# Kernel tuning notes

Measured on AMD Instinct MI355X. Metric: run time of the kernel, lower is better.

Reference implementation:

```python
import jax, jax.numpy as jnp
import numpy as np
import math

EMBED_DIM = 1024
MEMORY_DIM = 1024
MEMORY_SIZE = 2048
B, S = 8, 4096


def bitnet_linear(x, W, b):
    """Eval-mode BitNetLinear: 1.58-bit weight quant + 8-bit activation quant."""
    w_scale = jnp.mean(jnp.abs(W))
    qW = jnp.sign(W) * (jnp.abs(W) > 0.5 * w_scale).astype(W.dtype)
    i_scale = jnp.max(jnp.abs(x)) / 127.0
    qx = jnp.clip(jnp.round(x / i_scale), -128.0, 127.0)
    out = jnp.einsum('bsi,oi->bso', qx, qW) * (w_scale * i_scale)
    return out + b


def setup_inputs() -> dict:
    key = jax.random.key(0)
    ks = jax.random.split(key, 9)
    return {
        'x': jax.random.normal(ks[0], (B, S, EMBED_DIM), jnp.float32),
        'memory_keys': jax.random.normal(ks[1], (MEMORY_SIZE, MEMORY_DIM), jnp.float32),
        'memory_values': jax.random.normal(ks[2], (MEMORY_SIZE, EMBED_DIM), jnp.float32),
        'Wk': jax.random.normal(ks[3], (MEMORY_DIM, EMBED_DIM), jnp.float32) * 0.1,
        'bk': jnp.zeros((MEMORY_DIM,), jnp.float32),
        'Wv': jax.random.normal(ks[4], (EMBED_DIM, EMBED_DIM), jnp.float32) * 0.1,
        'bv': jnp.zeros((EMBED_DIM,), jnp.float32),
        'Wo': jax.random.normal(ks[5], (EMBED_DIM, EMBED_DIM), jnp.float32) * 0.1,
        'bo': jnp.zeros((EMBED_DIM,), jnp.float32),
    }


def reference(x, memory_keys, memory_values, Wk, bk, Wv, bv, Wo, bo):
    # quantized key/value projections
    query_keys = bitnet_linear(x, Wk, bk)          # [B, S, Dm]
    _query_values = bitnet_linear(x, Wv, bv)       # computed in original (used only by update path)
    # memory cross-attention over fixed bank
    similarities = jnp.einsum('bsd,md->bsm', query_keys, memory_keys)  # [B, S, M]
    attention_weights = jax.nn.softmax(similarities / math.sqrt(MEMORY_DIM), axis=-1)
    retrieved = jnp.einsum('bsm,me->bse', attention_weights, memory_values)  # [B, S, E]
    output = bitnet_linear(x + retrieved, Wo, bo)
    return output
```

## Files before the change

### kernel.cpp

```cpp
#include <hip/hip_runtime.h>
#include <hip/hip_bf16.h>
#include <stdint.h>
#include <type_traits>

typedef __attribute__((ext_vector_type(8))) short bf16x8;
typedef __attribute__((ext_vector_type(4))) float f32x4;
typedef __attribute__((ext_vector_type(4))) int i32x4;

struct Scalars {
  double sum_wk;
  double sum_wo;
  unsigned int max_x_bits;
  unsigned int max_y_bits;
};

__device__ __forceinline__ unsigned short f2bf(float f) {
  __hip_bfloat16 h = __float2bfloat16(f);
  return *reinterpret_cast<unsigned short*>(&h);
}

__device__ __forceinline__ void async16(void* lds, const void* g) {
  __builtin_amdgcn_global_load_lds((__attribute__((address_space(1))) void*)g,
                                   (__attribute__((address_space(3))) void*)lds, 16, 0, 0);
}

__device__ __forceinline__ void tile_swizzle(int nxShift, int& bx, int& by) {
  const int per = gridDim.x >> 3;
  const int tile = (blockIdx.x & 7) * per + (blockIdx.x >> 3);
  bx = tile & ((1 << nxShift) - 1);
  by = tile >> nxShift;
}

__device__ __forceinline__ f32x4 mm(bf16x8 a, bf16x8 b, f32x4 c) {
  return __builtin_amdgcn_mfma_f32_16x16x32_bf16(a, b, c, 0, 0, 0);
}
__device__ __forceinline__ i32x4 mm(i32x4 a, i32x4 b, i32x4 c) {
  return __builtin_amdgcn_mfma_i32_16x16x64_i8(a, b, c, 0, 0, 0);
}

__global__ __launch_bounds__(256) void stats_kernel(const float* __restrict__ Wk,
                                                    const float* __restrict__ Wo,
                                                    const float* __restrict__ x,
                                                    const float* __restrict__ bk,
                                                    const float* __restrict__ mk,
                                                    float* __restrict__ bias2,
                                                    Scalars* __restrict__ sc) {
  const int which = blockIdx.y;
  size_t tid = (size_t)blockIdx.x * 256 + threadIdx.x;
  size_t stride = (size_t)gridDim.x * 256;
  if (which < 2) {
    const float* w = which ? Wo : Wk;
    const size_t n = 1048576;
    double s = 0.0;
    for (size_t i = tid * 4; i < n; i += stride * 4) {
      float4 v = *(const float4*)(w + i);
      s += (double)fabsf(v.x) + (double)fabsf(v.y) + (double)fabsf(v.z) + (double)fabsf(v.w);
    }
#pragma unroll
    for (int o = 32; o > 0; o >>= 1) s += __shfl_xor(s, o);
    __shared__ double sm[4];
    if ((threadIdx.x & 63) == 0) sm[threadIdx.x >> 6] = s;
    __syncthreads();
    if (threadIdx.x == 0)
      atomicAdd(which ? &sc->sum_wo : &sc->sum_wk, sm[0] + sm[1] + sm[2] + sm[3]);
  } else if (which == 2) {
    const size_t n = (size_t)32768 * 1024;
    float m = 0.0f;
    for (size_t i = tid * 4; i < n; i += stride * 4) {
      float4 v = *(const float4*)(x + i);
      m = fmaxf(m, fmaxf(fmaxf(fabsf(v.x), fabsf(v.y)), fmaxf(fabsf(v.z), fabsf(v.w))));
    }
#pragma unroll
    for (int o = 32; o > 0; o >>= 1) m = fmaxf(m, __shfl_xor(m, o));
    __shared__ float smf[4];
    if ((threadIdx.x & 63) == 0) smf[threadIdx.x >> 6] = m;
    __syncthreads();
    if (threadIdx.x == 0)
      atomicMax(&sc->max_x_bits,
                __float_as_uint(fmaxf(fmaxf(smf[0], smf[1]), fmaxf(smf[2], smf[3]))));
  } else {
    if (blockIdx.x >= 512) return;
    const int l = threadIdx.x & 63, wv = threadIdx.x >> 6;
    const int m = blockIdx.x * 4 + wv;
    float dot = 0.f;
#pragma unroll
    for (int c = 0; c < 4; ++c) {
      float4 b4 = *(const float4*)(bk + c * 256 + l * 4);
      float4 k4 = *(const float4*)(mk + (size_t)m * 1024 + c * 256 + l * 4);
      dot += b4.x * k4.x + b4.y * k4.y + b4.z * k4.z + b4.w * k4.w;
    }
#pragma unroll
    for (int o = 32; o > 0; o >>= 1) dot += __shfl_xor(dot, o);
    if (l == 0) bias2[m] = dot * 0.03125f;
  }
}

__global__ __launch_bounds__(256) void prep_kernel(
    const float* __restrict__ Wk, const float* __restrict__ Wo,
    const float* __restrict__ mk, const float* __restrict__ mv,
    const float* __restrict__ x, __hip_bfloat16* __restrict__ qWkT,
    char* __restrict__ qWo8, __hip_bfloat16* __restrict__ mkb,
    __hip_bfloat16* __restrict__ mvT, __hip_bfloat16* __restrict__ qxb,
    const Scalars* __restrict__ sc) {
  __shared__ float tl[32][33];
  const int which = blockIdx.y;
  const int t = threadIdx.x;
  size_t tid = (size_t)blockIdx.x * 256 + t;
  size_t stride = (size_t)gridDim.x * 256;
  if (which == 0) {
    if (blockIdx.x >= 1024) return;
    const float thr = 0.5f * (float)(sc->sum_wk * (1.0 / 1048576.0));
    const int ti = blockIdx.x & 31;
    const int tj = blockIdx.x >> 5;
    const int tx = t & 31, ty = t >> 5;
#pragma unroll
    for (int r = 0; r < 4; ++r)
      tl[ty + r * 8][tx] = Wk[(size_t)(tj * 32 + ty + r * 8) * 1024 + ti * 32 + tx];
    __syncthreads();
#pragma unroll
    for (int r = 0; r < 4; ++r) {
      float v = tl[tx][ty + r * 8];
      float q = fabsf(v) > thr ? (v > 0.f ? 1.f : -1.f) : 0.f;
      qWkT[(size_t)(ti * 32 + ty + r * 8) * 1024 + tj * 32 + tx] = __float2bfloat16(q);
    }
  } else if (which == 1) {
    const double sum = sc->sum_wo;
    const float thr = 0.5f * (float)(sum * (1.0 / 1048576.0));
    const size_t n = 1048576;
    for (size_t i = tid * 4; i < n; i += stride * 4) {
      float4 v = *(const float4*)(Wo + i);
      char4 o;
      o.x = (char)(fabsf(v.x) > thr ? (v.x > 0.f ? 1 : -1) : 0);
      o.y = (char)(fabsf(v.y) > thr ? (v.y > 0.f ? 1 : -1) : 0);
      o.z = (char)(fabsf(v.z) > thr ? (v.z > 0.f ? 1 : -1) : 0);
      o.w = (char)(fabsf(v.w) > thr ? (v.w > 0.f ? 1 : -1) : 0);
      *(char4*)(qWo8 + i) = o;
    }
  } else if (which == 2) {
    const size_t n = (size_t)2048 * 1024;
    for (size_t i = tid * 4; i < n; i += stride * 4) {
      float4 v = *(const float4*)(mk + i);
      ushort4 o;
      o.x = f2bf(v.x); o.y = f2bf(v.y); o.z = f2bf(v.z); o.w = f2bf(v.w);
      *(ushort4*)((unsigned short*)mkb + i) = o;
    }
  } else if (which == 3) {
    const int ti = blockIdx.x & 31;
    const int tj = blockIdx.x >> 5;
    const int tx = t & 31, ty = t >> 5;
#pragma unroll
    for (int r = 0; r < 4; ++r)
      tl[ty + r * 8][tx] = mv[(size_t)(tj * 32 + ty + r * 8) * 1024 + ti * 32 + tx];
    __syncthreads();
#pragma unroll
    for (int r = 0; r < 4; ++r)
      mvT[(size_t)(ti * 32 + ty + r * 8) * 2048 + tj * 32 + tx] =
          __float2bfloat16(tl[tx][ty + r * 8]);
  } else {
    const float isc = __uint_as_float(sc->max_x_bits) / 127.0f;
    const size_t n = (size_t)32768 * 1024;
    for (size_t i = tid * 4; i < n; i += stride * 4) {
      float4 v = *(const float4*)(x + i);
      ushort4 o;
      o.x = f2bf(fminf(fmaxf(rintf(v.x / isc), -128.f), 127.f));
      o.y = f2bf(fminf(fmaxf(rintf(v.y / isc), -128.f), 127.f));
      o.z = f2bf(fminf(fmaxf(rintf(v.z / isc), -128.f), 127.f));
      o.w = f2bf(fminf(fmaxf(rintf(v.w / isc), -128.f), 127.f));
      *(ushort4*)((unsigned short*)qxb + i) = o;
    }
  }
}

__global__ __launch_bounds__(256) void quant_act_bf16_kernel(
    const __hip_bfloat16* __restrict__ y, char* __restrict__ q,
    const unsigned int* __restrict__ maxbits, size_t n) {
  const float isc = __uint_as_float(*maxbits) / 127.0f;
  size_t tid = (size_t)blockIdx.x * blockDim.x + threadIdx.x;
  size_t stride = (size_t)gridDim.x * blockDim.x;
  for (size_t i = tid * 8; i < n; i += stride * 8) {
    uint4 r = *(const uint4*)((const unsigned short*)y + i);
    float v[8];
    v[0] = __uint_as_float(r.x << 16); v[1] = __uint_as_float(r.x & 0xffff0000u);
    v[2] = __uint_as_float(r.y << 16); v[3] = __uint_as_float(r.y & 0xffff0000u);
    v[4] = __uint_as_float(r.z << 16); v[5] = __uint_as_float(r.z & 0xffff0000u);
    v[6] = __uint_as_float(r.w << 16); v[7] = __uint_as_float(r.w & 0xffff0000u);
    char o[8];
#pragma unroll
    for (int j = 0; j < 8; ++j)
      o[j] = (char)(int)fminf(fmaxf(rintf(v[j] / isc), -128.f), 127.f);
    uint2 pk;
    pk.x = (unsigned char)o[0] | ((unsigned)(unsigned char)o[1] << 8) |
           ((unsigned)(unsigned char)o[2] << 16) | ((unsigned)(unsigned char)o[3] << 24);
    pk.y = (unsigned char)o[4] | ((unsigned)(unsigned char)o[5] << 8) |
           ((unsigned)(unsigned char)o[6] << 16) | ((unsigned)(unsigned char)o[7] << 24);
    *(uint2*)(q + i) = pk;
  }
}

__global__ __launch_bounds__(256) void softmax_kernel(__hip_bfloat16* __restrict__ sims) {
  const int t = threadIdx.x, l = t & 63, wv = t >> 6;
  unsigned short* row = (unsigned short*)(sims + ((size_t)blockIdx.x * 4 + wv) * 2048);
  uint4 r4[4];
  float v[32];
#pragma unroll
  for (int c = 0; c < 4; ++c) r4[c] = *(const uint4*)(row + c * 512 + l * 8);
#pragma unroll
  for (int c = 0; c < 4; ++c) {
    unsigned u0 = r4[c].x, u1 = r4[c].y, u2 = r4[c].z, u3 = r4[c].w;
    v[c * 8 + 0] = __uint_as_float(u0 << 16); v[c * 8 + 1] = __uint_as_float(u0 & 0xffff0000u);
    v[c * 8 + 2] = __uint_as_float(u1 << 16); v[c * 8 + 3] = __uint_as_float(u1 & 0xffff0000u);
    v[c * 8 + 4] = __uint_as_float(u2 << 16); v[c * 8 + 5] = __uint_as_float(u2 & 0xffff0000u);
    v[c * 8 + 6] = __uint_as_float(u3 << 16); v[c * 8 + 7] = __uint_as_float(u3 & 0xffff0000u);
  }
  float m = v[0];
#pragma unroll
  for (int i = 1; i < 32; ++i) m = fmaxf(m, v[i]);
#pragma unroll
  for (int o = 32; o > 0; o >>= 1) m = fmaxf(m, __shfl_xor(m, o));
  float s = 0.f;
#pragma unroll
  for (int i = 0; i < 32; ++i) { v[i] = expf(v[i] - m); s += v[i]; }
#pragma unroll
  for (int o = 32; o > 0; o >>= 1) s += __shfl_xor(s, o);
#pragma unroll
  for (int c = 0; c < 4; ++c) {
    unsigned short b[8];
#pragma unroll
    for (int j = 0; j < 8; ++j) b[j] = f2bf(v[c * 8 + j] / s);
    uint4 o4;
    o4.x = (unsigned)b[0] | ((unsigned)b[1] << 16);
    o4.y = (unsigned)b[2] | ((unsigned)b[3] << 16);
    o4.z = (unsigned)b[4] | ((unsigned)b[5] << 16);
    o4.w = (unsigned)b[6] | ((unsigned)b[7] << 16);
    *(uint4*)(row + c * 512 + l * 8) = o4;
  }
}

#define CFENCE() asm volatile("" ::: "memory")
#define BAR8() { CFENCE(); __builtin_amdgcn_s_barrier(); CFENCE(); }
#define WLGKM(N) { asm volatile("s_waitcnt lgkmcnt(" #N ")" ::: "memory"); __builtin_amdgcn_sched_barrier(0); }
#define WVM(N) asm volatile("s_waitcnt vmcnt(" #N ")" ::: "memory")

template <int EPI>
__global__ __launch_bounds__(512, 2) void gemm8(
    const char* __restrict__ A, const char* __restrict__ B, void* __restrict__ C,
    const float* __restrict__ aux, Scalars* __restrict__ sc,
    int Ndim, int KB, int nxShift) {
  constexpr bool I8 = (EPI == 4);
  using FR  = typename std::conditional<I8, i32x4, bf16x8>::type;
  using ACC = typename std::conditional<I8, i32x4, f32x4>::type;
  __shared__ __align__(16) char lds[4][2][16384];

  int bx, by;
  tile_swizzle(nxShift, bx, by);
  const int rowBlk = by * 256, colBlk = bx * 256;

  const int t = threadIdx.x, w = t >> 6, l = t & 63;
  const int wm = w >> 2, wn = w & 3;
  const int quad = l >> 4, m16 = l & 15;
  const int NT = KB >> 7, NIT = NT >> 1;

  int voA[2][2], voB[2][2];
#pragma unroll
  for (int hf = 0; hf < 2; ++hf)
#pragma unroll
    for (int j = 0; j < 2; ++j) {
      const int idx = j * 64 + (t >> 3);
      const int kby = ((t & 7) ^ (idx & 7)) << 4;
      voA[hf][j] = (rowBlk + ((idx >> 6) << 7) + (hf << 6) + (idx & 63)) * KB + kby;
      voB[hf][j] = (colBlk + ((idx >> 5) << 6) + (hf << 5) + (idx & 31)) * KB + kby;
    }

  const char* baA[2];
  const char* baB[2];
#pragma unroll
  for (int ks = 0; ks < 2; ++ks) {
    const int x16 = ((ks << 6) + (quad << 4)) ^ ((m16 & 7) << 4);
    baA[ks] = &lds[0][0][(wm * 64 + m16) * 128 + x16];
    baB[ks] = &lds[2][0][(wn * 32 + m16) * 128 + x16];
  }

#define STG_A(slot, hf, tk)                                                         \
  if ((tk) < NT) {                                                                  \
    _Pragma("unroll") for (int j = 0; j < 2; ++j)                                   \
      async16(&lds[hf][slot][j * 8192 + (w << 10)],                                 \
              A + (((size_t)(tk)) << 7) + voA[hf][j]);                              \
  }
#define STG_B(slot, hf, tk)                                                         \
  if ((tk) < NT) {                                                                  \
    _Pragma("unroll") for (int j = 0; j < 2; ++j)                                   \
      async16(&lds[2 + (hf)][slot][j * 8192 + (w << 10)],                           \
              B + (((size_t)(tk)) << 7) + voB[hf][j]);                              \
  }

#define LD_A(dst, slot, hf, f, ks) \
  dst = *(const FR*)(baA[ks] + ((hf)*32768 + (slot)*16384 + (f)*2048));
#define LD_B(dst, slot, hf, gg, ks) \
  dst = *(const FR*)(baB[ks] + ((hf)*32768 + (slot)*16384 + (gg)*2048));

#define R_A0(s) { _Pragma("unroll") for (int f_ = 0; f_ < 4; ++f_) { LD_A(af[f_][0], s, 0, f_, 0); LD_A(af[f_][1], s, 0, f_, 1); } }
#define R_A1(s) { _Pragma("unroll") for (int f_ = 0; f_ < 4; ++f_) { LD_A(af[f_][0], s, 1, f_, 0); LD_A(af[f_][1], s, 1, f_, 1); } }
#define R_B0(s) { _Pragma("unroll") for (int g_ = 0; g_ < 2; ++g_) { LD_B(b0[g_][0], s, 0, g_, 0); LD_B(b0[g_][1], s, 0, g_, 1); } }
#define R_B1(s) { _Pragma("unroll") for (int g_ = 0; g_ < 2; ++g_) { LD_B(b1[g_][0], s, 1, g_, 0); LD_B(b1[g_][1], s, 1, g_, 1); } }

#define MM8(FO, GO, BR)                                                             \
  __builtin_amdgcn_s_setprio(1);                                                    \
  _Pragma("unroll") for (int f_ = 0; f_ < 4; ++f_)                                  \
    _Pragma("unroll") for (int g_ = 0; g_ < 2; ++g_) {                              \
      acc[(FO) + f_][(GO) + g_] = mm(af[f_][0], BR[g_][0], acc[(FO) + f_][(GO) + g_]); \
      acc[(FO) + f_][(GO) + g_] = mm(af[f_][1], BR[g_][1], acc[(FO) + f_][(GO) + g_]); \
    }                                                                               \
  __builtin_amdgcn_s_setprio(0);

#define TSTEP(s, tk, last)                                                          \
  {                                                                                 \
    R_B1(s);                                                                        \
    STG_A((s) ^ 1, 1, (tk) + 1);                                                    \
    BAR8(); WLGKM(4);                                                               \
    MM8(0, 0, b0);                                                                  \
    BAR8();                                                                         \
    STG_A(s, 0, (tk) + 2);                                                          \
    BAR8(); WLGKM(0);                                                               \
    MM8(0, 2, b1);                                                                  \
    R_A1(s);                                                                        \
    BAR8();                                                                         \
    STG_B(s, 0, (tk) + 2);                                                          \
    BAR8(); WLGKM(0);                                                               \
    MM8(4, 0, b0);                                                                  \
    BAR8();                                                                         \
    STG_B(s, 1, (tk) + 2);                                                          \
    if (last) { WVM(0); } else { WVM(6); }                                          \
    BAR8();                                                                         \
    MM8(4, 2, b1);                                                                  \
    R_A0((s) ^ 1);                                                                  \
    R_B0((s) ^ 1);                                                                  \
  }

  FR af[4][2], b0[2][2], b1[2][2];
  ACC acc[8][4] = {};

  STG_A(0, 0, 0); STG_B(0, 0, 0); STG_B(0, 1, 0); STG_A(0, 1, 0);
  CFENCE();
  STG_A(1, 0, 1); STG_B(1, 0, 1); STG_B(1, 1, 1);
  WVM(6);
  BAR8();
  R_A0(0); R_B0(0);

  for (int it = 0; it < NIT; ++it) {
    const bool last = (it == NIT - 1);
    TSTEP(0, it * 2, last);
    TSTEP(1, it * 2 + 1, last);
  }

  float sK = 0.0f;
  if constexpr (EPI == 5)
    sK = (float)(sc->sum_wk * (1.0 / 1048576.0)) *
         (__uint_as_float(sc->max_x_bits) / 127.0f) * 0.03125f;
  if constexpr (EPI == 4)
    sK = (float)(sc->sum_wo * (1.0 / 1048576.0)) * (__uint_as_float(sc->max_y_bits) / 127.0f);

  float amax = 0.0f;
#pragma unroll
  for (int f = 0; f < 8; ++f) {
#pragma unroll
    for (int g = 0; g < 4; ++g) {
      const int col = colBlk + wn * 64 + g * 16 + m16;
#pragma unroll
      for (int rg = 0; rg < 4; ++rg) {
        const int row = rowBlk + wm * 128 + f * 16 + quad * 4 + rg;
        if constexpr (EPI == 1) {
          ((__hip_bfloat16*)C)[(size_t)row * Ndim + col] =
              __float2bfloat16(acc[f][g][rg] + aux[col]);
        } else if constexpr (EPI == 2) {
          float v = acc[f][g][rg] + aux[(size_t)row * Ndim + col];
          ((__hip_bfloat16*)C)[(size_t)row * Ndim + col] = __float2bfloat16(v);
          amax = fmaxf(amax, fabsf(v));
        } else if constexpr (EPI == 5) {
          ((__hip_bfloat16*)C)[(size_t)row * Ndim + col] =
              __float2bfloat16(acc[f][g][rg] * sK);
        } else {
          ((float*)C)[(size_t)row * Ndim + col] = (float)acc[f][g][rg] * sK + aux[col];
        }
      }
    }
  }

  if constexpr (EPI == 2) {
#pragma unroll
    for (int o = 32; o > 0; o >>= 1) amax = fmaxf(amax, __shfl_xor(amax, o));
    if (l == 0) atomicMax(&sc->max_y_bits, __float_as_uint(amax));
  }
#undef STG_A
#undef STG_B
#undef LD_A
#undef LD_B
#undef R_A0
#undef R_A1
#undef R_B0
#undef R_B1
#undef MM8
#undef TSTEP
}

extern "C" void kernel_launch(void* const* d_in, const int* in_sizes, int n_in,
                              void* d_out, int out_size, void* d_ws, size_t ws_size,
                              hipStream_t stream) {
  (void)in_sizes; (void)n_in; (void)out_size; (void)ws_size;
  const float* x  = (const float*)d_in[0];
  const float* mk = (const float*)d_in[1];
  const float* mv = (const float*)d_in[2];
  const float* Wk = (const float*)d_in[3];
  const float* bk = (const float*)d_in[4];
  const float* Wo = (const float*)d_in[7];
  const float* bo = (const float*)d_in[8];
  float* out = (float*)d_out;

  const int M = 32768, E = 1024, MEM = 2048;

  char* ws = (char*)d_ws;
  Scalars* sc = (Scalars*)ws;
  const size_t off0 = 256;
  __hip_bfloat16* qxb = (__hip_bfloat16*)(ws + off0);
  __hip_bfloat16* yb  = (__hip_bfloat16*)(ws + off0);
  const size_t off1 = off0 + (size_t)M * E * 2;
  __hip_bfloat16* sims = (__hip_bfloat16*)(ws + off1);
  char* qy8 = (char*)sims;
  const size_t off2 = off1 + (size_t)M * MEM * 2;
  __hip_bfloat16* qWkT = (__hip_bfloat16*)(ws + off2);
  char* qWo8 = (char*)(qWkT + (size_t)E * E);
  __hip_bfloat16* mkb = (__hip_bfloat16*)(qWo8 + (size_t)E * E);
  __hip_bfloat16* mvT = mkb + (size_t)MEM * E;
  __hip_bfloat16* K2b = mvT + (size_t)E * MEM;
  float* bias2 = (float*)(K2b + (size_t)MEM * E);

  hipMemsetAsync(ws, 0, 256, stream);

  stats_kernel<<<dim3(1024, 4), dim3(256), 0, stream>>>(Wk, Wo, x, bk, mk, bias2, sc);
  prep_kernel<<<dim3(2048, 5), dim3(256), 0, stream>>>(Wk, Wo, mk, mv, x, qWkT, qWo8,
                                                       mkb, mvT, qxb, sc);

  gemm8<5><<<dim3((E / 256) * (MEM / 256)), dim3(512), 0, stream>>>(
      (const char*)mkb, (const char*)qWkT, K2b, nullptr, sc, E, 2 * E, 2);
  gemm8<1><<<dim3((MEM / 256) * (M / 256)), dim3(512), 0, stream>>>(
      (const char*)qxb, (const char*)K2b, sims, bias2, sc, MEM, 2 * E, 3);
  softmax_kernel<<<dim3(M / 4), dim3(256), 0, stream>>>(sims);
  gemm8<2><<<dim3((E / 256) * (M / 256)), dim3(512), 0, stream>>>(
      (const char*)sims, (const char*)mvT, yb, x, sc, E, 2 * MEM, 2);
  quant_act_bf16_kernel<<<dim3(2048), dim3(256), 0, stream>>>(yb, qy8, &sc->max_y_bits,
                                                              (size_t)M * E);
  gemm8<4><<<dim3((E / 256) * (M / 256)), dim3(512), 0, stream>>>(
      (const char*)qy8, (const char*)qWo8, out, bo, sc, E, E, 2);
}
```

Baseline: 737.7 us.

## Split-K the small memory-key projection GEMM with a separate reduction kernel

The 2048x1024x1024 GEMM that builds K2 only launched 32 tiles, far fewer than the number of CUs. It now launches 256 blocks that each handle one eighth of K and write fp32 partial results to a workspace buffer. A new kernel then sums the eight partials, applies the scale and converts to bf16. This gains parallelism on a small GEMM at the cost of an extra launch and roughly 64MB of partial-sum traffic.

New measurement: 727.3 us. No clear change (-1.4%).

```diff
diff --git a/kernel.cpp b/kernel.cpp
--- a/kernel.cpp
+++ b/kernel.cpp
@@ -171,6 +171,23 @@
   }
 }
 
+__global__ __launch_bounds__(256) void k2red_kernel(const float* __restrict__ K2f,
+                                                    __hip_bfloat16* __restrict__ K2b,
+                                                    const Scalars* __restrict__ sc) {
+  const float sK = (float)(sc->sum_wk * (1.0 / 1048576.0)) *
+                   (__uint_as_float(sc->max_x_bits) / 127.0f) * 0.03125f;
+  const size_t i = ((size_t)blockIdx.x * 256 + threadIdx.x) * 4;
+  float4 s = {0.f, 0.f, 0.f, 0.f};
+#pragma unroll
+  for (int p = 0; p < 8; ++p) {
+    float4 v = *(const float4*)(K2f + (size_t)p * 2097152 + i);
+    s.x += v.x; s.y += v.y; s.z += v.z; s.w += v.w;
+  }
+  ushort4 o;
+  o.x = f2bf(s.x * sK); o.y = f2bf(s.y * sK); o.z = f2bf(s.z * sK); o.w = f2bf(s.w * sK);
+  *(ushort4*)((unsigned short*)K2b + i) = o;
+}
+
 __global__ __launch_bounds__(256) void quant_act_bf16_kernel(
     const __hip_bfloat16* __restrict__ y, char* __restrict__ q,
     const unsigned int* __restrict__ maxbits, size_t n) {
@@ -252,13 +269,23 @@
   __shared__ __align__(16) char lds[4][2][16384];
 
   int bx, by;
-  tile_swizzle(nxShift, bx, by);
+  if constexpr (EPI == 6) {
+    const int split = blockIdx.x & 7;
+    const int tile = blockIdx.x >> 3;
+    bx = tile & 3; by = tile >> 2;
+    A += (size_t)split << 8;
+    B += (size_t)split << 8;
+    C = (void*)((char*)C + ((size_t)split << 23));
+  } else {
+    tile_swizzle(nxShift, bx, by);
+  }
   const int rowBlk = by * 256, colBlk = bx * 256;
 
   const int t = threadIdx.x, w = t >> 6, l = t & 63;
   const int wm = w >> 2, wn = w & 3;
   const int quad = l >> 4, m16 = l & 15;
-  const int NT = KB >> 7, NIT = NT >> 1;
+  const int NT = (EPI == 6) ? 2 : (KB >> 7);
+  const int NIT = NT >> 1;
 
   int voA[2][2], voB[2][2];
 #pragma unroll
@@ -347,15 +374,12 @@
   R_A0(0); R_B0(0);
 
   for (int it = 0; it < NIT; ++it) {
-    const bool last = (it == NIT - 1);
+    const bool last = (it * 2 >= NT - 2);
     TSTEP(0, it * 2, last);
     TSTEP(1, it * 2 + 1, last);
   }
 
   float sK = 0.0f;
-  if constexpr (EPI == 5)
-    sK = (float)(sc->sum_wk * (1.0 / 1048576.0)) *
-         (__uint_as_float(sc->max_x_bits) / 127.0f) * 0.03125f;
   if constexpr (EPI == 4)
     sK = (float)(sc->sum_wo * (1.0 / 1048576.0)) * (__uint_as_float(sc->max_y_bits) / 127.0f);
 
@@ -375,9 +399,8 @@
           float v = acc[f][g][rg] + aux[(size_t)row * Ndim + col];
           ((__hip_bfloat16*)C)[(size_t)row * Ndim + col] = __float2bfloat16(v);
           amax = fmaxf(amax, fabsf(v));
-        } else if constexpr (EPI == 5) {
-          ((__hip_bfloat16*)C)[(size_t)row * Ndim + col] =
-              __float2bfloat16(acc[f][g][rg] * sK);
+        } else if constexpr (EPI == 6) {
+          ((float*)C)[(size_t)row * Ndim + col] = acc[f][g][rg];
         } else {
           ((float*)C)[(size_t)row * Ndim + col] = (float)acc[f][g][rg] * sK + aux[col];
         }
@@ -432,6 +455,7 @@
   __hip_bfloat16* mvT = mkb + (size_t)MEM * E;
   __hip_bfloat16* K2b = mvT + (size_t)E * MEM;
   float* bias2 = (float*)(K2b + (size_t)MEM * E);
+  float* K2f = bias2 + 2048;
 
   hipMemsetAsync(ws, 0, 256, stream);
 
@@ -439,8 +463,9 @@
   prep_kernel<<<dim3(2048, 5), dim3(256), 0, stream>>>(Wk, Wo, mk, mv, x, qWkT, qWo8,
                                                        mkb, mvT, qxb, sc);
 
-  gemm8<5><<<dim3((E / 256) * (MEM / 256)), dim3(512), 0, stream>>>(
-      (const char*)mkb, (const char*)qWkT, K2b, nullptr, sc, E, 2 * E, 2);
+  gemm8<6><<<dim3(256), dim3(512), 0, stream>>>(
+      (const char*)mkb, (const char*)qWkT, K2f, nullptr, sc, E, 2 * E, 0);
+  k2red_kernel<<<dim3(2048), dim3(256), 0, stream>>>(K2f, K2b, sc);
   gemm8<1><<<dim3((MEM / 256) * (M / 256)), dim3(512), 0, stream>>>(
       (const char*)qxb, (const char*)K2b, sims, bias2, sc, MEM, 2 * E, 3);
   softmax_kernel<<<dim3(M / 4), dim3(256), 0, stream>>>(sims);
```
